# Performance work log

Hardware: AMD Instinct MI355X
Metric: run time of the kernel (lower is better)

Reference implementation:

```python
import jax, jax.numpy as jnp
import numpy as np

B, TQ, TK, F_DIM = 8, 1024, 2048, 1024


def setup_inputs() -> dict:
    key = jax.random.key(0)
    ks = jax.random.split(key, 7)
    inputs = jax.random.normal(ks[0], (B, TQ, F_DIM), dtype=jnp.float32)
    features = jax.random.normal(ks[1], (B, TK, F_DIM), dtype=jnp.float32)
    # key-padding mask: each batch element has a valid encoder length in [TK//2, TK]
    lengths = jax.random.randint(ks[2], (B, 1, 1), TK // 2, TK + 1)
    features_mask = jnp.broadcast_to(jnp.arange(TK)[None, None, :] < lengths, (B, TQ, TK))
    # nn.init.normal_(weight, 0, 0.01); bias = 0
    Wq = 0.01 * jax.random.normal(ks[3], (F_DIM, F_DIM), dtype=jnp.float32)
    Wk = 0.01 * jax.random.normal(ks[4], (F_DIM, F_DIM), dtype=jnp.float32)
    Wv = 0.01 * jax.random.normal(ks[5], (F_DIM, F_DIM), dtype=jnp.float32)
    bq = jnp.zeros((F_DIM,), dtype=jnp.float32)
    bk = jnp.zeros((F_DIM,), dtype=jnp.float32)
    bv = jnp.zeros((F_DIM,), dtype=jnp.float32)
    scale = jnp.asarray(1.0 / np.sqrt(F_DIM), dtype=jnp.float32)  # learned scalar param
    return {"inputs": inputs, "features": features, "features_mask": features_mask,
            "Wq": Wq, "bq": bq, "Wk": Wk, "bk": bk, "Wv": Wv, "bv": bv, "scale": scale}


def reference(inputs, features, features_mask, Wq, bq, Wk, bk, Wv, bv, scale):
    # Q/K/V projections (torch Linear: x @ W.T + b)
    q = jnp.einsum('bqf,df->bqd', inputs, Wq) + bq      # [B,Tq,F]
    k = jnp.einsum('bkf,df->bkd', features, Wk) + bk    # [B,Tk,F]
    v = jnp.einsum('bkf,df->bkd', features, Wv) + bv    # [B,Tk,F]
    scores = jnp.einsum('bqd,bkd->bqk', q, k) * scale   # [B,Tq,Tk]
    scores = jnp.where(features_mask, scores, -jnp.inf)
    weights = jax.nn.softmax(scores, axis=-1)           # [B,Tq,Tk]
    # original: (values.unsqueeze(1) * weights.unsqueeze(3)).sum(2) == weights @ v
    context = jnp.einsum('bqk,bkd->bqd', weights, v)    # [B,Tq,F]
    return context, weights[:, None, :, :]              # weights: [B,1,Tq,Tk]
```

## Files before the change

### kernel.cpp

```cpp
#include <hip/hip_runtime.h>
#include <hip/hip_bf16.h>

typedef unsigned short u16;
typedef __attribute__((ext_vector_type(8))) short bf16x8;
typedef __attribute__((ext_vector_type(4))) float f32x4;
typedef __attribute__((ext_vector_type(4))) u16 u16x4;

__device__ inline u16 f2bf(float f) {
  unsigned int x = __float_as_uint(f);
  unsigned int r = x + 0x7fffu + ((x >> 16) & 1u);
  return (u16)(r >> 16);
}

__device__ inline void gload16(const u16* g, u16* l) {
  __builtin_amdgcn_global_load_lds(
      (const __attribute__((address_space(1))) void*)g,
      (__attribute__((address_space(3))) void*)l, 16, 0, 0);
}

__global__ __launch_bounds__(256) void cvt_kernel(const float* __restrict__ in,
                                                  u16* __restrict__ out, long n4) {
  long i = (long)blockIdx.x * 256 + threadIdx.x;
  long stride = (long)gridDim.x * 256;
  for (; i < n4; i += stride) {
    float4 f = ((const float4*)in)[i];
    u16x4 u;
    u[0] = f2bf(f.x); u[1] = f2bf(f.y); u[2] = f2bf(f.z); u[3] = f2bf(f.w);
    ((u16x4*)out)[i] = u;
  }
}

__global__ __launch_bounds__(256) void lengths_kernel(const void* __restrict__ mask,
                                                      int* __restrict__ lengths,
                                                      int TQ_, int TK_) {
  int b = blockIdx.x;
  unsigned int first = *(const unsigned int*)mask;
  int mode;
  if (first == 1u) mode = 0;
  else if (first == 0x01010101u) mode = 1;
  else if (first == 0x3f800000u) mode = 2;
  else mode = 1;
  long base = (long)b * TQ_ * TK_;
  int cnt = 0;
  for (int k = threadIdx.x; k < TK_; k += blockDim.x) {
    bool nz;
    if (mode == 0)      nz = ((const int*)mask)[base + k] != 0;
    else if (mode == 2) nz = ((const float*)mask)[base + k] != 0.f;
    else                nz = ((const unsigned char*)mask)[base + k] != 0;
    cnt += nz ? 1 : 0;
  }
#pragma unroll
  for (int o = 32; o > 0; o >>= 1) cnt += __shfl_xor(cnt, o);
  __shared__ int red[4];
  int wv = threadIdx.x >> 6, lane = threadIdx.x & 63;
  if (lane == 0) red[wv] = cnt;
  __syncthreads();
  if (threadIdx.x == 0) lengths[b] = red[0] + red[1] + red[2] + red[3];
}

template <int MODE>
__global__ __launch_bounds__(256) void gemm_bt(
    const u16* __restrict__ A, long sA,
    const u16* __restrict__ Bm, long sB,
    void* __restrict__ Out, long sO,
    const float* __restrict__ bias,
    const float* __restrict__ scale_ptr,
    const int* __restrict__ lengths,
    int M, int N, int K) {
  __shared__ u16 lA[128 * 32];
  __shared__ u16 lB[128 * 32];
  int tid = threadIdx.x;
  int w = tid >> 6, lane = tid & 63;
  int bx = blockIdx.x, by = blockIdx.y, z = blockIdx.z;
  const u16* A_ = A + (size_t)z * sA + (size_t)by * 128 * K;
  const u16* B_ = Bm + (size_t)z * sB + (size_t)bx * 128 * K;
  int wm = (w >> 1) * 64, wn = (w & 1) * 64;
  int lm = lane >> 4, ln = lane & 15;

  f32x4 acc[4][4] = {};

  int c0 = w * 2, c1 = w * 2 + 1;
  int off0 = c0 * 1024 + lane * 16;
  int off1 = c1 * 1024 + lane * 16;
  const u16* ga0 = A_ + (size_t)(off0 >> 6) * K + ((off0 & 63) >> 1);
  const u16* ga1 = A_ + (size_t)(off1 >> 6) * K + ((off1 & 63) >> 1);
  const u16* gb0 = B_ + (size_t)(off0 >> 6) * K + ((off0 & 63) >> 1);
  const u16* gb1 = B_ + (size_t)(off1 >> 6) * K + ((off1 & 63) >> 1);

  int nk = K >> 5;
  for (int kb = 0; kb < nk; ++kb) {
    gload16(ga0, &lA[c0 * 512]);
    gload16(ga1, &lA[c1 * 512]);
    gload16(gb0, &lB[c0 * 512]);
    gload16(gb1, &lB[c1 * 512]);
    ga0 += 32; ga1 += 32; gb0 += 32; gb1 += 32;
    __syncthreads();
    bf16x8 af[4], bfr[4];
#pragma unroll
    for (int mi = 0; mi < 4; ++mi)
      af[mi] = *(const bf16x8*)&lA[(wm + mi * 16 + ln) * 32 + lm * 8];
#pragma unroll
    for (int ni = 0; ni < 4; ++ni)
      bfr[ni] = *(const bf16x8*)&lB[(wn + ni * 16 + ln) * 32 + lm * 8];
#pragma unroll
    for (int mi = 0; mi < 4; ++mi)
#pragma unroll
      for (int ni = 0; ni < 4; ++ni)
        acc[mi][ni] = __builtin_amdgcn_mfma_f32_16x16x32_bf16(af[mi], bfr[ni],
                                                              acc[mi][ni], 0, 0, 0);
    __syncthreads();
  }

  float scl = 0.f;
  int len = 0;
  if (MODE == 2) { scl = *scale_ptr; len = lengths[z]; }

#pragma unroll
  for (int mi = 0; mi < 4; ++mi) {
#pragma unroll
    for (int ni = 0; ni < 4; ++ni) {
      int r0 = by * 128 + wm + mi * 16 + lm * 4;
      int c = bx * 128 + wn + ni * 16 + ln;
      f32x4 v = acc[mi][ni];
      if (MODE == 0) {
        float bval = bias[c];
        u16* o = (u16*)Out + (size_t)z * sO;
#pragma unroll
        for (int r = 0; r < 4; ++r) o[(size_t)(r0 + r) * N + c] = f2bf(v[r] + bval);
      } else if (MODE == 1) {
        float bval = bias[c];
        u16* o = (u16*)Out + (size_t)z * sO;
        u16x4 pk;
#pragma unroll
        for (int r = 0; r < 4; ++r) pk[r] = f2bf(v[r] + bval);
        *(u16x4*)&o[(size_t)c * M + r0] = pk;
      } else if (MODE == 2) {
        float* o = (float*)Out + (size_t)z * sO;
#pragma unroll
        for (int r = 0; r < 4; ++r) {
          float val = v[r] * scl;
          if (c >= len) val = -INFINITY;
          o[(size_t)(r0 + r) * N + c] = val;
        }
      } else {
        float* o = (float*)Out + (size_t)z * sO;
#pragma unroll
        for (int r = 0; r < 4; ++r) o[(size_t)(r0 + r) * N + c] = v[r];
      }
    }
  }
}

__global__ __launch_bounds__(256) void softmax_kernel(float* __restrict__ W,
                                                      u16* __restrict__ P, int TK_) {
  size_t row = blockIdx.x;
  float* wr = W + row * (size_t)TK_;
  u16* pr = P + row * (size_t)TK_;
  int t = threadIdx.x;
  int wv = t >> 6, lane = t & 63;
  float4 a = *(const float4*)&wr[t * 4];
  float4 c = *(const float4*)&wr[1024 + t * 4];
  float m = fmaxf(fmaxf(fmaxf(a.x, a.y), fmaxf(a.z, a.w)),
                  fmaxf(fmaxf(c.x, c.y), fmaxf(c.z, c.w)));
#pragma unroll
  for (int o = 32; o > 0; o >>= 1) m = fmaxf(m, __shfl_xor(m, o));
  __shared__ float red[4];
  if (lane == 0) red[wv] = m;
  __syncthreads();
  m = fmaxf(fmaxf(red[0], red[1]), fmaxf(red[2], red[3]));
  float e0 = __expf(a.x - m), e1 = __expf(a.y - m), e2 = __expf(a.z - m), e3 = __expf(a.w - m);
  float e4 = __expf(c.x - m), e5 = __expf(c.y - m), e6 = __expf(c.z - m), e7 = __expf(c.w - m);
  float s = e0 + e1 + e2 + e3 + e4 + e5 + e6 + e7;
#pragma unroll
  for (int o = 32; o > 0; o >>= 1) s += __shfl_xor(s, o);
  __syncthreads();
  if (lane == 0) red[wv] = s;
  __syncthreads();
  s = red[0] + red[1] + red[2] + red[3];
  float inv = 1.0f / s;
  float4 oa = make_float4(e0 * inv, e1 * inv, e2 * inv, e3 * inv);
  float4 ob = make_float4(e4 * inv, e5 * inv, e6 * inv, e7 * inv);
  *(float4*)&wr[t * 4] = oa;
  *(float4*)&wr[1024 + t * 4] = ob;
  u16x4 pa, pb;
  pa[0] = f2bf(oa.x); pa[1] = f2bf(oa.y); pa[2] = f2bf(oa.z); pa[3] = f2bf(oa.w);
  pb[0] = f2bf(ob.x); pb[1] = f2bf(ob.y); pb[2] = f2bf(ob.z); pb[3] = f2bf(ob.w);
  *(u16x4*)&pr[t * 4] = pa;
  *(u16x4*)&pr[1024 + t * 4] = pb;
}

extern "C" void kernel_launch(void* const* d_in, const int* in_sizes, int n_in,
                              void* d_out, int out_size, void* d_ws, size_t ws_size,
                              hipStream_t stream) {
  const int B_ = 8, TQ_ = 1024, TK_ = 2048, F_ = 1024;
  const float* inputs = (const float*)d_in[0];
  const float* features = (const float*)d_in[1];
  const void* mask = d_in[2];
  const float* Wq = (const float*)d_in[3];
  const float* bq = (const float*)d_in[4];
  const float* Wk = (const float*)d_in[5];
  const float* bk = (const float*)d_in[6];
  const float* Wv = (const float*)d_in[7];
  const float* bv = (const float*)d_in[8];
  const float* scale = (const float*)d_in[9];

  char* ws = (char*)d_ws;
  size_t o = 0;
  auto alloc = [&](size_t bytes) {
    size_t r = o;
    o += (bytes + 255) & ~(size_t)255;
    return r;
  };
  u16* inB = (u16*)(ws + alloc((size_t)B_ * TQ_ * F_ * 2));
  u16* ftB = (u16*)(ws + alloc((size_t)B_ * TK_ * F_ * 2));
  u16* wqB = (u16*)(ws + alloc((size_t)F_ * F_ * 2));
  u16* wkB = (u16*)(ws + alloc((size_t)F_ * F_ * 2));
  u16* wvB = (u16*)(ws + alloc((size_t)F_ * F_ * 2));
  u16* Qb = (u16*)(ws + alloc((size_t)B_ * TQ_ * F_ * 2));
  u16* Kb = (u16*)(ws + alloc((size_t)B_ * TK_ * F_ * 2));
  u16* Vt = (u16*)(ws + alloc((size_t)B_ * F_ * TK_ * 2));
  u16* P = (u16*)(ws + alloc((size_t)B_ * TQ_ * TK_ * 2));
  int* lens = (int*)(ws + alloc(B_ * sizeof(int)));

  float* outCtx = (float*)d_out;
  float* outW = (float*)d_out + (size_t)B_ * TQ_ * F_;

  auto cvt = [&](const float* in, u16* out, long n) {
    long n4 = n / 4;
    long g = (n4 + 255) / 256;
    int grid = (int)(g < 2048 ? g : 2048);
    cvt_kernel<<<dim3(grid), dim3(256), 0, stream>>>(in, out, n4);
  };
  cvt(inputs, inB, (long)B_ * TQ_ * F_);
  cvt(features, ftB, (long)B_ * TK_ * F_);
  cvt(Wq, wqB, (long)F_ * F_);
  cvt(Wk, wkB, (long)F_ * F_);
  cvt(Wv, wvB, (long)F_ * F_);

  lengths_kernel<<<dim3(B_), dim3(256), 0, stream>>>(mask, lens, TQ_, TK_);

  gemm_bt<0><<<dim3(F_ / 128, (B_ * TQ_) / 128, 1), dim3(256), 0, stream>>>(
      inB, 0, wqB, 0, Qb, 0, bq, nullptr, nullptr, B_ * TQ_, F_, F_);
  gemm_bt<0><<<dim3(F_ / 128, (B_ * TK_) / 128, 1), dim3(256), 0, stream>>>(
      ftB, 0, wkB, 0, Kb, 0, bk, nullptr, nullptr, B_ * TK_, F_, F_);
  gemm_bt<1><<<dim3(F_ / 128, TK_ / 128, B_), dim3(256), 0, stream>>>(
      ftB, (long)TK_ * F_, wvB, 0, Vt, (long)F_ * TK_, bv, nullptr, nullptr,
      TK_, F_, F_);
  gemm_bt<2><<<dim3(TK_ / 128, TQ_ / 128, B_), dim3(256), 0, stream>>>(
      Qb, (long)TQ_ * F_, Kb, (long)TK_ * F_, outW, (long)TQ_ * TK_, nullptr,
      scale, lens, TQ_, TK_, F_);
  softmax_kernel<<<dim3(B_ * TQ_), dim3(256), 0, stream>>>(outW, P, TK_);
  gemm_bt<3><<<dim3(F_ / 128, TQ_ / 128, B_), dim3(256), 0, stream>>>(
      P, (long)TQ_ * TK_, Vt, (long)F_ * TK_, outCtx, (long)TQ_ * F_, nullptr,
      nullptr, nullptr, TQ_, F_, TK_);
}
```

Baseline: 523.6 us.

## Replace GEMM with 256x256 double-buffered 8-wave pipelined kernel with swizzled LDS

Replaces the simple 128x128 single-buffered bf16 GEMM with a 256x256 tile kernel using 8 waves, 64-wide K steps, and double-buffered LDS (128KB dynamic shared memory). Global-to-LDS loads for the next tile are interleaved with MFMA phases under explicit vmcnt waits, barriers, and setprio. It also adds XOR-swizzled LDS layout to avoid bank conflicts and a workgroup-ID remap for cache locality. The aim is to hide memory latency and raise MFMA utilisation, at the cost of larger tiles, more registers, and more complex synchronisation.

```diff
diff --git a/kernel.cpp b/kernel.cpp
--- a/kernel.cpp
+++ b/kernel.cpp
@@ -17,6 +17,10 @@
       (const __attribute__((address_space(1))) void*)g,
       (__attribute__((address_space(3))) void*)l, 16, 0, 0);
 }
+
+#define BAR() asm volatile("s_barrier" ::: "memory")
+#define VMCNT4() asm volatile("s_waitcnt vmcnt(4)" ::: "memory")
+#define VMCNT0() asm volatile("s_waitcnt vmcnt(0)" ::: "memory")
 
 __global__ __launch_bounds__(256) void cvt_kernel(const float* __restrict__ in,
                                                   u16* __restrict__ out, long n4) {
@@ -58,8 +62,28 @@
   if (threadIdx.x == 0) lengths[b] = red[0] + red[1] + red[2] + red[3];
 }
 
+#define DO_MFMA(pp)                                                                             \
+  __builtin_amdgcn_s_setprio(1);                                                                \
+  acc[(pp)*2+0][0] = __builtin_amdgcn_mfma_f32_16x16x32_bf16(af[0][0], bfr[0][0], acc[(pp)*2+0][0], 0, 0, 0); \
+  acc[(pp)*2+0][1] = __builtin_amdgcn_mfma_f32_16x16x32_bf16(af[0][0], bfr[1][0], acc[(pp)*2+0][1], 0, 0, 0); \
+  acc[(pp)*2+0][2] = __builtin_amdgcn_mfma_f32_16x16x32_bf16(af[0][0], bfr[2][0], acc[(pp)*2+0][2], 0, 0, 0); \
+  acc[(pp)*2+0][3] = __builtin_amdgcn_mfma_f32_16x16x32_bf16(af[0][0], bfr[3][0], acc[(pp)*2+0][3], 0, 0, 0); \
+  acc[(pp)*2+1][0] = __builtin_amdgcn_mfma_f32_16x16x32_bf16(af[1][0], bfr[0][0], acc[(pp)*2+1][0], 0, 0, 0); \
+  acc[(pp)*2+1][1] = __builtin_amdgcn_mfma_f32_16x16x32_bf16(af[1][0], bfr[1][0], acc[(pp)*2+1][1], 0, 0, 0); \
+  acc[(pp)*2+1][2] = __builtin_amdgcn_mfma_f32_16x16x32_bf16(af[1][0], bfr[2][0], acc[(pp)*2+1][2], 0, 0, 0); \
+  acc[(pp)*2+1][3] = __builtin_amdgcn_mfma_f32_16x16x32_bf16(af[1][0], bfr[3][0], acc[(pp)*2+1][3], 0, 0, 0); \
+  acc[(pp)*2+0][0] = __builtin_amdgcn_mfma_f32_16x16x32_bf16(af[0][1], bfr[0][1], acc[(pp)*2+0][0], 0, 0, 0); \
+  acc[(pp)*2+0][1] = __builtin_amdgcn_mfma_f32_16x16x32_bf16(af[0][1], bfr[1][1], acc[(pp)*2+0][1], 0, 0, 0); \
+  acc[(pp)*2+0][2] = __builtin_amdgcn_mfma_f32_16x16x32_bf16(af[0][1], bfr[2][1], acc[(pp)*2+0][2], 0, 0, 0); \
+  acc[(pp)*2+0][3] = __builtin_amdgcn_mfma_f32_16x16x32_bf16(af[0][1], bfr[3][1], acc[(pp)*2+0][3], 0, 0, 0); \
+  acc[(pp)*2+1][0] = __builtin_amdgcn_mfma_f32_16x16x32_bf16(af[1][1], bfr[0][1], acc[(pp)*2+1][0], 0, 0, 0); \
+  acc[(pp)*2+1][1] = __builtin_amdgcn_mfma_f32_16x16x32_bf16(af[1][1], bfr[1][1], acc[(pp)*2+1][1], 0, 0, 0); \
+  acc[(pp)*2+1][2] = __builtin_amdgcn_mfma_f32_16x16x32_bf16(af[1][1], bfr[2][1], acc[(pp)*2+1][2], 0, 0, 0); \
+  acc[(pp)*2+1][3] = __builtin_amdgcn_mfma_f32_16x16x32_bf16(af[1][1], bfr[3][1], acc[(pp)*2+1][3], 0, 0, 0); \
+  __builtin_amdgcn_s_setprio(0);
+
 template <int MODE>
-__global__ __launch_bounds__(256) void gemm_bt(
+__global__ __launch_bounds__(512, 2) void gemm8p(
     const u16* __restrict__ A, long sA,
     const u16* __restrict__ Bm, long sB,
     void* __restrict__ Out, long sO,
@@ -67,60 +91,122 @@
     const float* __restrict__ scale_ptr,
     const int* __restrict__ lengths,
     int M, int N, int K) {
-  __shared__ u16 lA[128 * 32];
-  __shared__ u16 lB[128 * 32];
-  int tid = threadIdx.x;
-  int w = tid >> 6, lane = tid & 63;
-  int bx = blockIdx.x, by = blockIdx.y, z = blockIdx.z;
-  const u16* A_ = A + (size_t)z * sA + (size_t)by * 128 * K;
-  const u16* B_ = Bm + (size_t)z * sB + (size_t)bx * 128 * K;
-  int wm = (w >> 1) * 64, wn = (w & 1) * 64;
-  int lm = lane >> 4, ln = lane & 15;
-
-  f32x4 acc[4][4] = {};
-
-  int c0 = w * 2, c1 = w * 2 + 1;
-  int off0 = c0 * 1024 + lane * 16;
-  int off1 = c1 * 1024 + lane * 16;
-  const u16* ga0 = A_ + (size_t)(off0 >> 6) * K + ((off0 & 63) >> 1);
-  const u16* ga1 = A_ + (size_t)(off1 >> 6) * K + ((off1 & 63) >> 1);
-  const u16* gb0 = B_ + (size_t)(off0 >> 6) * K + ((off0 & 63) >> 1);
-  const u16* gb1 = B_ + (size_t)(off1 >> 6) * K + ((off1 & 63) >> 1);
-
-  int nk = K >> 5;
-  for (int kb = 0; kb < nk; ++kb) {
-    gload16(ga0, &lA[c0 * 512]);
-    gload16(ga1, &lA[c1 * 512]);
-    gload16(gb0, &lB[c0 * 512]);
-    gload16(gb1, &lB[c1 * 512]);
-    ga0 += 32; ga1 += 32; gb0 += 32; gb1 += 32;
-    __syncthreads();
-    bf16x8 af[4], bfr[4];
-#pragma unroll
-    for (int mi = 0; mi < 4; ++mi)
-      af[mi] = *(const bf16x8*)&lA[(wm + mi * 16 + ln) * 32 + lm * 8];
-#pragma unroll
-    for (int ni = 0; ni < 4; ++ni)
-      bfr[ni] = *(const bf16x8*)&lB[(wn + ni * 16 + ln) * 32 + lm * 8];
-#pragma unroll
-    for (int mi = 0; mi < 4; ++mi)
-#pragma unroll
-      for (int ni = 0; ni < 4; ++ni)
-        acc[mi][ni] = __builtin_amdgcn_mfma_f32_16x16x32_bf16(af[mi], bfr[ni],
-                                                              acc[mi][ni], 0, 0, 0);
-    __syncthreads();
+  extern __shared__ __align__(16) u16 lds[];
+  const int tid = threadIdx.x;
+  const int w = tid >> 6, lane = tid & 63;
+  const int lm = lane >> 4, ln = lane & 15;
+  const int wm = w >> 2, wn = w & 3;
+
+  int gx = gridDim.x, gy = gridDim.y;
+  int nwg = gx * gy * gridDim.z;
+  int id = blockIdx.x + gx * (blockIdx.y + gy * blockIdx.z);
+  int cpx = nwg >> 3;
+  int swz = (id & 7) * cpx + (id >> 3);
+  int bx = swz % gx;
+  int tmp = swz / gx;
+  int by = tmp % gy;
+  int z = tmp / gy;
+
+  const u16* A_ = A + (size_t)z * sA + (size_t)by * 256 * K;
+  const u16* B_ = Bm + (size_t)z * sB + (size_t)bx * 256 * K;
+
+  int srcOff[2][2];
+#pragma unroll
+  for (int half = 0; half < 2; ++half)
+#pragma unroll
+    for (int l = 0; l < 2; ++l) {
+      int off = half * 16384 + l * 8192 + tid * 16;
+      int row = off >> 7;
+      int sb = (off & 127) ^ ((row & 7) << 4);
+      srcOff[half][l] = row * K + (sb >> 1);
+    }
+
+  const int aBase = (wm * 128 + ln) * 64;
+  const int bBase = (wn * 64 + ln) * 64;
+  const int swzk0 = ((0 + lm) ^ (ln & 7)) * 8;
+  const int swzk1 = ((4 + lm) ^ (ln & 7)) * 8;
+
+  f32x4 acc[8][4] = {};
+  bf16x8 af[2][2];
+  bf16x8 bfr[4][2];
+
+  auto stage = [&](const u16* gb, int slot, int isB, int half, int t) {
+#pragma unroll
+    for (int l = 0; l < 2; ++l)
+      gload16(gb + srcOff[half][l] + t * 64,
+              (u16*)((char*)&lds[0] + slot * 65536 + isB * 32768 + half * 16384 +
+                     l * 8192 + w * 1024));
+  };
+  auto ldA = [&](int slot, int pp) {
+#pragma unroll
+    for (int m2 = 0; m2 < 2; ++m2) {
+      af[m2][0] = *(const bf16x8*)&lds[slot * 32768 + aBase + (pp * 2 + m2) * 1024 + swzk0];
+      af[m2][1] = *(const bf16x8*)&lds[slot * 32768 + aBase + (pp * 2 + m2) * 1024 + swzk1];
+    }
+  };
+  auto ldB = [&](int slot) {
+#pragma unroll
+    for (int ni = 0; ni < 4; ++ni) {
+      bfr[ni][0] = *(const bf16x8*)&lds[slot * 32768 + 16384 + bBase + ni * 1024 + swzk0];
+      bfr[ni][1] = *(const bf16x8*)&lds[slot * 32768 + 16384 + bBase + ni * 1024 + swzk1];
+    }
+  };
+
+  stage(B_, 0, 1, 0, 0);
+  stage(B_, 0, 1, 1, 0);
+  stage(A_, 0, 0, 0, 0);
+  stage(A_, 0, 0, 1, 0);
+  stage(B_, 1, 1, 0, 1);
+  stage(B_, 1, 1, 1, 1);
+  VMCNT4();
+  BAR();
+
+  const int nt = K >> 6;
+  const int nIt = nt >> 1;
+  for (int it = 0; it < nIt; ++it) {
+    const int t = 2 * it;
+    const bool last = (it == nIt - 1);
+    ldB(0); ldA(0, 0);
+    stage(A_, 1, 0, 0, t + 1);
+    BAR(); DO_MFMA(0); BAR();
+    ldA(0, 1);
+    stage(A_, 1, 0, 1, t + 1);
+    if (!last) stage(B_, 0, 1, 0, t + 2);
+    BAR(); DO_MFMA(1); BAR();
+    ldA(0, 2);
+    if (!last) stage(B_, 0, 1, 1, t + 2);
+    BAR(); DO_MFMA(2); BAR();
+    ldA(0, 3);
+    BAR(); DO_MFMA(3);
+    if (!last) { VMCNT4(); } else { VMCNT0(); }
+    BAR();
+    ldB(1); ldA(1, 0);
+    if (!last) stage(A_, 0, 0, 0, t + 2);
+    BAR(); DO_MFMA(0); BAR();
+    ldA(1, 1);
+    if (!last) stage(A_, 0, 0, 1, t + 2);
+    BAR(); DO_MFMA(1); BAR();
+    ldA(1, 2);
+    if (!last) stage(B_, 1, 1, 0, t + 3);
+    BAR(); DO_MFMA(2); BAR();
+    ldA(1, 3);
+    if (!last) stage(B_, 1, 1, 1, t + 3);
+    BAR(); DO_MFMA(3);
+    if (!last) { VMCNT4(); }
+    BAR();
   }
 
   float scl = 0.f;
   int len = 0;
   if (MODE == 2) { scl = *scale_ptr; len = lengths[z]; }
-
-#pragma unroll
-  for (int mi = 0; mi < 4; ++mi) {
+  const int rowBase = by * 256 + wm * 128 + lm * 4;
+  const int colBase = bx * 256 + wn * 64 + ln;
+#pragma unroll
+  for (int mi = 0; mi < 8; ++mi) {
 #pragma unroll
     for (int ni = 0; ni < 4; ++ni) {
-      int r0 = by * 128 + wm + mi * 16 + lm * 4;
-      int c = bx * 128 + wn + ni * 16 + ln;
+      int r0 = rowBase + mi * 16;
+      int c = colBase + ni * 16;
       f32x4 v = acc[mi][ni];
       if (MODE == 0) {
         float bval = bias[c];
@@ -239,18 +325,27 @@
 
   lengths_kernel<<<dim3(B_), dim3(256), 0, stream>>>(mask, lens, TQ_, TK_);
 
-  gemm_bt<0><<<dim3(F_ / 128, (B_ * TQ_) / 128, 1), dim3(256), 0, stream>>>(
+  (void)hipFuncSetAttribute(reinterpret_cast<const void*>(&gemm8p<0>),
+                            hipFuncAttributeMaxDynamicSharedMemorySize, 131072);
+  (void)hipFuncSetAttribute(reinterpret_cast<const void*>(&gemm8p<1>),
+                            hipFuncAttributeMaxDynamicSharedMemorySize, 131072);
+  (void)hipFuncSetAttribute(reinterpret_cast<const void*>(&gemm8p<2>),
+                            hipFuncAttributeMaxDynamicSharedMemorySize, 131072);
+  (void)hipFuncSetAttribute(reinterpret_cast<const void*>(&gemm8p<3>),
+                            hipFuncAttributeMaxDynamicSharedMemorySize, 131072);
+
+  gemm8p<0><<<dim3(F_ / 256, (B_ * TQ_) / 256, 1), dim3(512), 131072, stream>>>(
       inB, 0, wqB, 0, Qb, 0, bq, nullptr, nullptr, B_ * TQ_, F_, F_);
-  gemm_bt<0><<<dim3(F_ / 128, (B_ * TK_) / 128, 1), dim3(256), 0, stream>>>(
+  gemm8p<0><<<dim3(F_ / 256, (B_ * TK_) / 256, 1), dim3(512), 131072, stream>>>(
       ftB, 0, wkB, 0, Kb, 0, bk, nullptr, nullptr, B_ * TK_, F_, F_);
-  gemm_bt<1><<<dim3(F_ / 128, TK_ / 128, B_), dim3(256), 0, stream>>>(
+  gemm8p<1><<<dim3(F_ / 256, TK_ / 256, B_), dim3(512), 131072, stream>>>(
       ftB, (long)TK_ * F_, wvB, 0, Vt, (long)F_ * TK_, bv, nullptr, nullptr,
       TK_, F_, F_);
-  gemm_bt<2><<<dim3(TK_ / 128, TQ_ / 128, B_), dim3(256), 0, stream>>>(
+  gemm8p<2><<<dim3(TK_ / 256, TQ_ / 256, B_), dim3(512), 131072, stream>>>(
       Qb, (long)TQ_ * F_, Kb, (long)TK_ * F_, outW, (long)TQ_ * TK_, nullptr,
       scale, lens, TQ_, TK_, F_);
   softmax_kernel<<<dim3(B_ * TQ_), dim3(256), 0, stream>>>(outW, P, TK_);
-  gemm_bt<3><<<dim3(F_ / 128, TQ_ / 128, B_), dim3(256), 0, stream>>>(
+  gemm8p<3><<<dim3(F_ / 256, TQ_ / 256, B_), dim3(512), 131072, stream>>>(
       P, (long)TQ_ * TK_, Vt, (long)F_ * TK_, outCtx, (long)TQ_ * F_, nullptr,
       nullptr, nullptr, TQ_, F_, TK_);
 }
```

Result: faster. 441.5 us (-15.7%).
